# Kernel tuning notes

Measured on AMD Instinct MI355X. Metric: run time of the kernel, lower is better.

Reference implementation:

```python
import jax, jax.numpy as jnp
import numpy as np

B, L, D, V1, V2, V3 = 512, 48, 256, 512, 512, 64


def setup_inputs() -> dict:
    key = jax.random.key(0)
    ks = jax.random.split(key, 20)
    def w(k, shape, fan_in):
        return jax.random.normal(k, shape, dtype=jnp.float32) / np.sqrt(fan_in)
    inp = {
        'x1': jax.random.normal(ks[0], (B, L, V1), dtype=jnp.float32),
        'x2': jax.random.normal(ks[1], (B, L, V2), dtype=jnp.float32),
        's': jax.random.normal(ks[2], (B, V3), dtype=jnp.float32),
        'w_e1': w(ks[3], (D, V1), V1), 'b_e1': jnp.zeros((D,), jnp.float32),
        'w_e2': w(ks[4], (D, V2), V2), 'b_e2': jnp.zeros((D,), jnp.float32),
        'w_s': w(ks[5], (D, V3), V3), 'b_s': jnp.zeros((D,), jnp.float32),
        'w_x': w(ks[6], (1, D), D),                      # mlp_for_x, no bias
        'w_h': w(ks[7], (L, D), D), 'b_h': w(ks[8], (L,), D),  # mlp_for_hidden
        'w_ih': w(ks[9], (3 * D, D), D), 'w_hh': w(ks[10], (3 * D, D), D),
        'b_ih': w(ks[11], (3 * D,), D), 'b_hh': w(ks[12], (3 * D,), D),
        'w_out': w(ks[13], (1, D), D), 'b_out': jnp.zeros((1,), jnp.float32),
    }
    return inp


def _gru_cell(x, h, w_ih, w_hh, b_ih, b_hh):
    # torch GRUCell: gates ordered r, z, n
    gi = x @ w_ih.T + b_ih
    gh = h @ w_hh.T + b_hh
    i_r, i_z, i_n = jnp.split(gi, 3, axis=-1)
    h_r, h_z, h_n = jnp.split(gh, 3, axis=-1)
    r = jax.nn.sigmoid(i_r + h_r)
    z = jax.nn.sigmoid(i_z + h_z)
    n = jnp.tanh(i_n + r * h_n)
    return (1.0 - z) * n + z * h


def reference(x1, x2, s, w_e1, b_e1, w_e2, b_e2, w_s, b_s, w_x, w_h, b_h,
              w_ih, w_hh, b_ih, b_hh, w_out, b_out):
    x1e = jax.nn.relu(jnp.einsum('blv,dv->bld', x1, w_e1) + b_e1)
    x2e = jax.nn.relu(jnp.einsum('blv,dv->bld', x2, w_e2) + b_e2)
    se = s @ w_s.T + b_s                      # [B, D]
    x = x1e + x2e                             # [B, L, D]
    # prefix[:, i] = sum_{j < i} x2e[:, j, 0]  (the torch.where zero test)
    cums = jnp.cumsum(x2e[:, :, 0], axis=1)
    prefix = jnp.concatenate([jnp.zeros((B, 1), x.dtype), cums[:, :-1]], axis=1)  # [B, L]
    idx = jnp.arange(L)

    def step(h, inputs):
        i, pref = inputs                       # i: scalar step, pref: [B]
        le = (idx <= i).astype(x.dtype)        # keep timesteps 0..i (pad rest with 0)
        ip = x * le[None, :, None]             # input_padded [B, L, D]
        lt = (idx < i)
        cond = (pref == 0.0)[:, None]          # batches with zero history in ch0
        guid = jnp.where(idx[None, :] == i, 1.0,
                         jnp.where(cond & lt[None, :], 1.0, 0.0)).astype(x.dtype)  # [B, L]
        gi = ip * guid[:, :, None]
        t1 = jnp.einsum('bld,d->bl', gi, w_x[0]) + (h @ w_h.T + b_h)  # [B, L]
        a = jax.nn.softmax(t1, axis=1)
        ctx = jnp.einsum('bld,bl->bd', ip, a)
        h2 = _gru_cell(ctx, h, w_ih, w_hh, b_ih, b_hh)
        return h2, None

    h0 = jnp.zeros((B, D), x.dtype)
    hF, _ = jax.lax.scan(step, h0, (idx, prefix.T))
    y = jax.nn.sigmoid((hF + se) @ w_out.T + b_out)  # [B, 1]
    return y
```

## Files before the change

### kernel.cpp

```cpp
#include <hip/hip_runtime.h>
#include <stdint.h>

#define B_ 512
#define L_ 48
#define D_ 256

typedef __attribute__((ext_vector_type(8))) short bf16x8;
typedef __attribute__((ext_vector_type(4))) short bf16x4;
typedef __attribute__((ext_vector_type(4))) float f32x4;
typedef __attribute__((ext_vector_type(4))) int i32x4;

__device__ __forceinline__ short f2bf(float f) {
    union { float f; unsigned u; } v; v.f = f;
    unsigned u = v.u;
    unsigned r = (u + 0x7FFFu + ((u >> 16) & 1u)) >> 16;
    return (short)r;
}
__device__ __forceinline__ float bf2f(short s) {
    union { unsigned u; float f; } v; v.u = ((unsigned)(unsigned short)s) << 16;
    return v.f;
}

__global__ __launch_bounds__(256) void k_prep(const float* __restrict__ w_hh,
                                              const float* __restrict__ w_h,
                                              const float* __restrict__ w_ih,
                                              signed char* __restrict__ W1q,
                                              signed char* __restrict__ W2q,
                                              float* __restrict__ qA,
                                              float* __restrict__ qC) {
    int w = threadIdx.x >> 6, lane = threadIdx.x & 63;
    int R = blockIdx.x * 4 + w;
    if (R >= 1584) return;
    const float* src;
    signed char* dst;
    bool isA = (R < 816);
    if (R < 768)      { src = w_hh + (size_t)R * 256;         dst = W1q + (size_t)R * 256; }
    else if (R < 816) { src = w_h + (size_t)(R - 768) * 256;  dst = W1q + (size_t)R * 256; }
    else              { src = w_ih + (size_t)(R - 816) * 256; dst = W2q + (size_t)(R - 816) * 256; }
    float4 v = *(const float4*)(src + lane * 4);
    float m = fmaxf(fmaxf(fabsf(v.x), fabsf(v.y)), fmaxf(fabsf(v.z), fabsf(v.w)));
    #pragma unroll
    for (int o = 32; o; o >>= 1) m = fmaxf(m, __shfl_xor(m, o));
    float sc = (m > 0.f) ? 127.f / m : 0.f;
    int b0 = __float2int_rn(v.x * sc), b1 = __float2int_rn(v.y * sc);
    int b2 = __float2int_rn(v.z * sc), b3 = __float2int_rn(v.w * sc);
    unsigned word = (unsigned)(b0 & 255) | ((unsigned)(b1 & 255) << 8) |
                    ((unsigned)(b2 & 255) << 16) | ((unsigned)(b3 & 255) << 24);
    ((unsigned*)dst)[lane] = word;
    if (lane == 0) {
        if (isA) qA[R] = m / (127.f * 127.f);
        else     qC[R - 816] = m * 8.f / (127.f * 127.f);
    }
}

__device__ __forceinline__ void gemm_pass(const float* __restrict__ X,
                                          const float* __restrict__ W,
                                          short (*sA)[40], short (*sB)[40],
                                          int m0, int n0, int srow, int sseg,
                                          int mf, int nf, int row16, int kg,
                                          f32x4 (&acc)[2][4]) {
    for (int k0 = 0; k0 < 512; k0 += 32) {
        __syncthreads();
        {
            const float* src = X + (size_t)(m0 + srow) * 512 + k0 + sseg * 8;
            float4 p0 = *(const float4*)(src);
            float4 p1 = *(const float4*)(src + 4);
            bf16x8 v;
            v[0] = f2bf(p0.x); v[1] = f2bf(p0.y); v[2] = f2bf(p0.z); v[3] = f2bf(p0.w);
            v[4] = f2bf(p1.x); v[5] = f2bf(p1.y); v[6] = f2bf(p1.z); v[7] = f2bf(p1.w);
            *(bf16x8*)&sA[srow][sseg * 8] = v;
        }
        {
            const float* src = W + (size_t)(n0 + srow) * 512 + k0 + sseg * 8;
            float4 p0 = *(const float4*)(src);
            float4 p1 = *(const float4*)(src + 4);
            bf16x8 v;
            v[0] = f2bf(p0.x); v[1] = f2bf(p0.y); v[2] = f2bf(p0.z); v[3] = f2bf(p0.w);
            v[4] = f2bf(p1.x); v[5] = f2bf(p1.y); v[6] = f2bf(p1.z); v[7] = f2bf(p1.w);
            *(bf16x8*)&sB[srow][sseg * 8] = v;
        }
        __syncthreads();
        bf16x8 a0 = *(bf16x8*)&sA[(mf + 0) * 16 + row16][kg * 8];
        bf16x8 a1 = *(bf16x8*)&sA[(mf + 1) * 16 + row16][kg * 8];
        #pragma unroll
        for (int j = 0; j < 4; ++j) {
            bf16x8 bv = *(bf16x8*)&sB[(nf + j) * 16 + row16][kg * 8];
            acc[0][j] = __builtin_amdgcn_mfma_f32_16x16x32_bf16(a0, bv, acc[0][j], 0, 0, 0);
            acc[1][j] = __builtin_amdgcn_mfma_f32_16x16x32_bf16(a1, bv, acc[1][j], 0, 0, 0);
        }
    }
}

__device__ __forceinline__ void gemm_pass_c0(const float* __restrict__ X,
                                             const float* __restrict__ W,
                                             const float* __restrict__ we2r0,
                                             bool doC0, float& c0acc,
                                             short (*sA)[40], short (*sB)[40],
                                             int m0, int n0, int srow, int sseg,
                                             int mf, int nf, int row16, int kg,
                                             f32x4 (&acc)[2][4]) {
    for (int k0 = 0; k0 < 512; k0 += 32) {
        __syncthreads();
        {
            const float* src = X + (size_t)(m0 + srow) * 512 + k0 + sseg * 8;
            float4 p0 = *(const float4*)(src);
            float4 p1 = *(const float4*)(src + 4);
            if (doC0) {
                const float* wr = we2r0 + k0 + sseg * 8;
                c0acc += p0.x * wr[0] + p0.y * wr[1] + p0.z * wr[2] + p0.w * wr[3]
                       + p1.x * wr[4] + p1.y * wr[5] + p1.z * wr[6] + p1.w * wr[7];
            }
            bf16x8 v;
            v[0] = f2bf(p0.x); v[1] = f2bf(p0.y); v[2] = f2bf(p0.z); v[3] = f2bf(p0.w);
            v[4] = f2bf(p1.x); v[5] = f2bf(p1.y); v[6] = f2bf(p1.z); v[7] = f2bf(p1.w);
            *(bf16x8*)&sA[srow][sseg * 8] = v;
        }
        {
            const float* src = W + (size_t)(n0 + srow) * 512 + k0 + sseg * 8;
            float4 p0 = *(const float4*)(src);
            float4 p1 = *(const float4*)(src + 4);
            bf16x8 v;
            v[0] = f2bf(p0.x); v[1] = f2bf(p0.y); v[2] = f2bf(p0.z); v[3] = f2bf(p0.w);
            v[4] = f2bf(p1.x); v[5] = f2bf(p1.y); v[6] = f2bf(p1.z); v[7] = f2bf(p1.w);
            *(bf16x8*)&sB[srow][sseg * 8] = v;
        }
        __syncthreads();
        bf16x8 a0 = *(bf16x8*)&sA[(mf + 0) * 16 + row16][kg * 8];
        bf16x8 a1 = *(bf16x8*)&sA[(mf + 1) * 16 + row16][kg * 8];
        #pragma unroll
        for (int j = 0; j < 4; ++j) {
            bf16x8 bv = *(bf16x8*)&sB[(nf + j) * 16 + row16][kg * 8];
            acc[0][j] = __builtin_amdgcn_mfma_f32_16x16x32_bf16(a0, bv, acc[0][j], 0, 0, 0);
            acc[1][j] = __builtin_amdgcn_mfma_f32_16x16x32_bf16(a1, bv, acc[1][j], 0, 0, 0);
        }
    }
}

__global__ __launch_bounds__(512) void k_embed(const float* __restrict__ x1,
                                               const float* __restrict__ x2,
                                               const float* __restrict__ w_e1,
                                               const float* __restrict__ b_e1,
                                               const float* __restrict__ w_e2,
                                               const float* __restrict__ b_e2,
                                               short* __restrict__ xb,
                                               float* __restrict__ c0) {
    __shared__ short sA[128][40];
    __shared__ short sB[128][40];
    int bid = blockIdx.x;
    int mt = bid >> 1, nt = bid & 1;
    int m0 = mt * 128, n0 = nt * 128;
    int tid = threadIdx.x;
    int lane = tid & 63, w = tid >> 6;
    int mf = (w & 3) * 2;
    int nf = (w >> 2) * 4;
    int row16 = lane & 15, kg = lane >> 4;
    int srow = tid >> 2, sseg = tid & 3;

    f32x4 acc[2][4], keep[2][4];
    #pragma unroll
    for (int a = 0; a < 2; ++a)
        #pragma unroll
        for (int j = 0; j < 4; ++j) { acc[a][j] = {0.f, 0.f, 0.f, 0.f}; }

    gemm_pass(x1, w_e1, sA, sB, m0, n0, srow, sseg, mf, nf, row16, kg, acc);
    #pragma unroll
    for (int a = 0; a < 2; ++a)
        #pragma unroll
        for (int j = 0; j < 4; ++j) { keep[a][j] = acc[a][j]; acc[a][j] = {0.f, 0.f, 0.f, 0.f}; }

    float c0acc = 0.f;
    const bool doC0 = (nt == 0);
    gemm_pass_c0(x2, w_e2, w_e2, doC0, c0acc, sA, sB, m0, n0, srow, sseg, mf, nf, row16, kg, acc);

    if (doC0) {
        float t = c0acc;
        t += __shfl_xor(t, 1);
        t += __shfl_xor(t, 2);
        if (sseg == 0) c0[m0 + srow] = fmaxf(t + b_e2[0], 0.f);
    }

    #pragma unroll
    for (int a = 0; a < 2; ++a) {
        int mbase = m0 + (mf + a) * 16 + kg * 4;
        #pragma unroll
        for (int j = 0; j < 4; ++j) {
            int n = n0 + (nf + j) * 16 + row16;
            float be1 = b_e1[n], be2 = b_e2[n];
            #pragma unroll
            for (int e = 0; e < 4; ++e) {
                float v1 = fmaxf(keep[a][j][e] + be1, 0.f);
                float v2 = fmaxf(acc[a][j][e] + be2, 0.f);
                xb[(size_t)(mbase + e) * 256 + n] = f2bf(v1 + v2);
            }
        }
    }
}

__global__ __launch_bounds__(256) void k_quant(const short* __restrict__ xb,
                                               const float* __restrict__ w_x,
                                               signed char* __restrict__ xq,
                                               float* __restrict__ xs,
                                               float* __restrict__ xw) {
    int w = threadIdx.x >> 6, lane = threadIdx.x & 63;
    int row = blockIdx.x * 4 + w;
    const short* src = xb + (size_t)row * 256 + lane * 4;
    bf16x4 v = *(const bf16x4*)src;
    float f0 = bf2f(v.x), f1 = bf2f(v.y), f2 = bf2f(v.z), f3 = bf2f(v.w);
    float m = fmaxf(fmaxf(f0, f1), fmaxf(f2, f3));
    float t = f0 * w_x[lane * 4] + f1 * w_x[lane * 4 + 1] +
              f2 * w_x[lane * 4 + 2] + f3 * w_x[lane * 4 + 3];
    #pragma unroll
    for (int o = 32; o; o >>= 1) {
        m = fmaxf(m, __shfl_xor(m, o));
        t += __shfl_xor(t, o);
    }
    float sc = (m > 0.f) ? 127.f / m : 0.f;
    int b0 = __float2int_rn(f0 * sc), b1 = __float2int_rn(f1 * sc);
    int b2 = __float2int_rn(f2 * sc), b3 = __float2int_rn(f3 * sc);
    unsigned word = (unsigned)(b0 & 255) | ((unsigned)(b1 & 255) << 8) |
                    ((unsigned)(b2 & 255) << 16) | ((unsigned)(b3 & 255) << 24);
    ((unsigned*)xq)[(size_t)row * 64 + lane] = word;
    if (lane == 0) { xs[row] = m / 127.f; xw[row] = t; }
}

__global__ __launch_bounds__(256) void k_aux2(const float* __restrict__ c0,
                                              const float* __restrict__ s_in,
                                              const float* __restrict__ w_s,
                                              const float* __restrict__ b_s,
                                              unsigned long long* __restrict__ condbits,
                                              float* __restrict__ se) {
    __shared__ float sS[64];
    int b = blockIdx.x;
    int t = threadIdx.x;
    if (t < 64) sS[t] = s_in[b * 64 + t];
    __syncthreads();
    float acc = b_s[t];
    const float* wr = w_s + t * 64;
    #pragma unroll 8
    for (int kk = 0; kk < 64; ++kk) acc += sS[kk] * wr[kk];
    se[(size_t)b * 256 + t] = acc;
    if (t == 0) {
        unsigned long long bits = 0;
        bool run = true;
        const float* cr = c0 + (size_t)b * 48;
        for (int i = 0; i < 48; ++i) {
            if (run) bits |= (1ull << i);
            run = run && (cr[i] == 0.0f);
        }
        condbits[b] = bits;
    }
}

__device__ __forceinline__ void mfma4r(const i32x4 (&a)[4], const i32x4 (&b)[4], i32x4& acc) {
    #pragma unroll
    for (int s = 0; s < 4; ++s)
        acc = __builtin_amdgcn_mfma_i32_16x16x64_i8(a[s], b[s], acc, 0, 0, 0);
}

__global__ __launch_bounds__(512, 1) void k_scan(const signed char* __restrict__ W1q,
                                                 const signed char* __restrict__ W2q,
                                                 const float* __restrict__ qAg,
                                                 const float* __restrict__ qCg,
                                                 const float* __restrict__ b_hh,
                                                 const float* __restrict__ b_h,
                                                 const float* __restrict__ b_ih,
                                                 const signed char* __restrict__ xq,
                                                 const float* __restrict__ xs,
                                                 const float* __restrict__ xw,
                                                 const unsigned long long* __restrict__ condbits,
                                                 const float* __restrict__ se,
                                                 const float* __restrict__ w_out,
                                                 const float* __restrict__ b_out,
                                                 float* __restrict__ out) {
    __shared__ signed char lWc[8][3][4096];
    __shared__ signed char lWs[3][4096];
    __shared__ signed char lXqT[2][256][52];
    __shared__ signed char lH8[16][272];
    __shared__ signed char lX8[16][272];
    __shared__ float lTw[8][52];
    __shared__ float lbA[816], lqA[816], lbC[768], lqC[768];
    __shared__ float lRed[8][2];

    const int tid = threadIdx.x;
    const int w = tid >> 6, lane = tid & 63;
    const int row16 = lane & 15, kg = lane >> 4;
    const int b0 = blockIdx.x * 2;
    const int g1 = 8 + w;
    const int c0 = w * 16 + row16, c1 = g1 * 16 + row16;
    const int swz = (row16 & 7) << 4;
    const float CS = 127.f / 8.f;
    const int mb = w >> 2;
    const int dimb = ((w & 3) << 6) + lane;

    for (int t = tid; t < 816; t += 512) {
        lbA[t] = (t < 768) ? b_hh[t] : b_h[t - 768];
        lqA[t] = qAg[t];
    }
    for (int t = tid; t < 768; t += 512) { lbC[t] = b_ih[t]; lqC[t] = qCg[t]; }
    for (int t = tid; t < 1088; t += 512) {
        ((int*)lH8)[t] = 0;
        ((int*)lX8)[t] = 0;
    }
    {
        int bq = tid >> 8, dq = tid & 255;
        const signed char* src = xq + (size_t)(b0 + bq) * 12288 + dq;
        signed char* dst = &lXqT[bq][dq][0];
        #pragma unroll
        for (int j = 0; j < 48; ++j) dst[j] = src[(size_t)j * 256];
    }

    const float xwv = (lane < 48) ? xw[(size_t)(b0 + mb) * 48 + lane] : 0.f;
    const float xsv = (lane < 48) ? xs[(size_t)(b0 + mb) * 48 + lane] : 0.f;
    const float qsv = (lane < 48) ? qAg[768 + lane] : 0.f;
    const float bsv = (lane < 48) ? b_h[lane] : 0.f;
    const unsigned long long cbits = condbits[b0 + mb];

    const int fro = row16 * 256 + kg * 16;
    i32x4 wa0[3][4], wa1[3][4], wc0[3][4];
    #pragma unroll
    for (int t = 0; t < 3; ++t) {
        const signed char* p0 = W1q + (size_t)(t * 16 + w) * 4096 + fro;
        const signed char* p1 = W1q + (size_t)(t * 16 + g1) * 4096 + fro;
        const signed char* p2 = W2q + (size_t)(t * 16 + w) * 4096 + fro;
        #pragma unroll
        for (int s = 0; s < 4; ++s) {
            wa0[t][s] = *(const i32x4*)(p0 + s * 64);
            wa1[t][s] = *(const i32x4*)(p1 + s * 64);
            wc0[t][s] = *(const i32x4*)(p2 + s * 64);
        }
    }
    #pragma unroll
    for (int t = 0; t < 3; ++t) {
        const signed char* src = W2q + (size_t)(t * 16 + g1) * 4096 + fro;
        signed char* dst = &lWc[w][t][row16 * 256];
        #pragma unroll
        for (int s = 0; s < 4; ++s)
            *(i32x4*)(dst + ((kg * 16 + s * 64) ^ swz)) = *(const i32x4*)(src + s * 64);
    }
    if (w < 3) {
        const signed char* src = W1q + (size_t)(48 + w) * 4096 + fro;
        signed char* dst = &lWs[w][row16 * 256];
        #pragma unroll
        for (int s = 0; s < 4; ++s)
            *(i32x4*)(dst + ((kg * 16 + s * 64) ^ swz)) = *(const i32x4*)(src + s * 64);
    }
    __syncthreads();

    float h0[2] = {0.f, 0.f};
    float h1[2] = {0.f, 0.f};

    for (int i = 0; i < 48; ++i) {
        i32x4 av[4];
        #pragma unroll
        for (int s = 0; s < 4; ++s) av[s] = *(const i32x4*)(&lH8[row16][0] + kg * 16 + s * 64);
        i32x4 sv0 = {0,0,0,0}, sv1 = {0,0,0,0}, sv2 = {0,0,0,0};
        #pragma unroll
        for (int s = 0; s < 4; ++s) {
            int off = (kg * 16 + s * 64) ^ swz;
            i32x4 q0 = *(const i32x4*)(&lWs[0][row16 * 256] + off);
            i32x4 q1 = *(const i32x4*)(&lWs[1][row16 * 256] + off);
            i32x4 q2 = *(const i32x4*)(&lWs[2][row16 * 256] + off);
            sv0 = __builtin_amdgcn_mfma_i32_16x16x64_i8(av[s], q0, sv0, 0, 0, 0);
            sv1 = __builtin_amdgcn_mfma_i32_16x16x64_i8(av[s], q1, sv1, 0, 0, 0);
            sv2 = __builtin_amdgcn_mfma_i32_16x16x64_i8(av[s], q2, sv2, 0, 0, 0);
        }
        i32x4 aR0 = {0,0,0,0}, aZ0 = {0,0,0,0}, aN0 = {0,0,0,0};
        i32x4 aR1 = {0,0,0,0}, aZ1 = {0,0,0,0}, aN1 = {0,0,0,0};
        mfma4r(av, wa0[0], aR0); mfma4r(av, wa0[1], aZ0); mfma4r(av, wa0[2], aN0);
        mfma4r(av, wa1[0], aR1); mfma4r(av, wa1[1], aZ1); mfma4r(av, wa1[2], aN1);

        {
            float e00 = (float)sv0[0], e10 = (float)sv0[1];
            float e01 = (float)sv1[0], e11 = (float)sv1[1];
            float e02 = (float)sv2[0], e12 = (float)sv2[1];
            float s0 = mb ? e10 : e00;
            float s1 = mb ? e11 : e01;
            float s2 = mb ? e12 : e02;
            float v0 = __shfl(s0, row16);
            float v1 = __shfl(s1, row16);
            float v2 = __shfl(s2, row16);
            float raw = (lane < 16) ? v0 : ((lane < 32) ? v1 : v2);
            float val = -3.0e38f;
            if (lane < 48) {
                val = raw * qsv + bsv;
                bool cb = (cbits >> i) & 1ull;
                if (lane == i || (cb && lane < i)) val += xwv;
            }
            float mx = val;
            #pragma unroll
            for (int o = 32; o; o >>= 1) mx = fmaxf(mx, __shfl_xor(mx, o));
            float ex = (lane < 48) ? __expf(val - mx) : 0.f;
            float sm = ex;
            #pragma unroll
            for (int o = 32; o; o >>= 1) sm += __shfl_xor(sm, o);
            if (lane < 48) lTw[w][lane] = (ex / sm) * xsv;
        }
        {
            const float* tw = lTw[w];
            const signed char* xv = &lXqT[mb][dimb][0];
            float acc = 0.f;
            int j = 0;
            for (; j + 3 <= i; j += 4) {
                union { int v; signed char c[4]; } pk;
                pk.v = *(const int*)(xv + j);
                float4 t4 = *(const float4*)(tw + j);
                acc += t4.x * (float)pk.c[0] + t4.y * (float)pk.c[1]
                     + t4.z * (float)pk.c[2] + t4.w * (float)pk.c[3];
            }
            for (; j <= i; ++j) acc += tw[j] * (float)xv[j];
            lX8[mb][dimb] = (signed char)__float2int_rn(fminf(fmaxf(acc * CS, -127.f), 127.f));
        }
        __syncthreads();

        i32x4 cv[4];
        #pragma unroll
        for (int s = 0; s < 4; ++s) cv[s] = *(const i32x4*)(&lX8[row16][0] + kg * 16 + s * 64);
        {
            i32x4 cr = {0,0,0,0}, cz = {0,0,0,0}, cn = {0,0,0,0};
            mfma4r(cv, wc0[0], cr); mfma4r(cv, wc0[1], cz); mfma4r(cv, wc0[2], cn);
            #pragma unroll
            for (int e = 0; e < 2; ++e) {
                float gr = (float)aR0[e] * lqA[c0]       + lbA[c0]       + (float)cr[e] * lqC[c0]       + lbC[c0];
                float gz = (float)aZ0[e] * lqA[256 + c0] + lbA[256 + c0] + (float)cz[e] * lqC[256 + c0] + lbC[256 + c0];
                float gh = (float)aN0[e] * lqA[512 + c0] + lbA[512 + c0];
                float gn = (float)cn[e] * lqC[512 + c0]  + lbC[512 + c0];
                float r = 1.f / (1.f + __expf(-gr));
                float z = 1.f / (1.f + __expf(-gz));
                float nn = 1.f - 2.f / (__expf(2.f * (gn + r * gh)) + 1.f);
                float hp = (1.f - z) * nn + z * h0[e];
                h0[e] = hp;
                if (kg == 0)
                    lH8[e][c0] = (signed char)__float2int_rn(fminf(fmaxf(hp, -1.f), 1.f) * 127.f);
            }
        }
        {
            i32x4 cr = {0,0,0,0}, cz = {0,0,0,0}, cn = {0,0,0,0};
            #pragma unroll
            for (int s = 0; s < 4; ++s) {
                int off = (kg * 16 + s * 64) ^ swz;
                i32x4 br = *(const i32x4*)(&lWc[w][0][row16 * 256] + off);
                i32x4 bz = *(const i32x4*)(&lWc[w][1][row16 * 256] + off);
                i32x4 bn = *(const i32x4*)(&lWc[w][2][row16 * 256] + off);
                cr = __builtin_amdgcn_mfma_i32_16x16x64_i8(cv[s], br, cr, 0, 0, 0);
                cz = __builtin_amdgcn_mfma_i32_16x16x64_i8(cv[s], bz, cz, 0, 0, 0);
                cn = __builtin_amdgcn_mfma_i32_16x16x64_i8(cv[s], bn, cn, 0, 0, 0);
            }
            #pragma unroll
            for (int e = 0; e < 2; ++e) {
                float gr = (float)aR1[e] * lqA[c1]       + lbA[c1]       + (float)cr[e] * lqC[c1]       + lbC[c1];
                float gz = (float)aZ1[e] * lqA[256 + c1] + lbA[256 + c1] + (float)cz[e] * lqC[256 + c1] + lbC[256 + c1];
                float gh = (float)aN1[e] * lqA[512 + c1] + lbA[512 + c1];
                float gn = (float)cn[e] * lqC[512 + c1]  + lbC[512 + c1];
                float r = 1.f / (1.f + __expf(-gr));
                float z = 1.f / (1.f + __expf(-gz));
                float nn = 1.f - 2.f / (__expf(2.f * (gn + r * gh)) + 1.f);
                float hp = (1.f - z) * nn + z * h1[e];
                h1[e] = hp;
                if (kg == 0)
                    lH8[e][c1] = (signed char)__float2int_rn(fminf(fmaxf(hp, -1.f), 1.f) * 127.f);
            }
        }
        __syncthreads();
    }

    if (kg == 0) {
        float p[2];
        #pragma unroll
        for (int e = 0; e < 2; ++e) {
            int b = b0 + e;
            p[e] = (h0[e] + se[(size_t)b * 256 + c0]) * w_out[c0]
                 + (h1[e] + se[(size_t)b * 256 + c1]) * w_out[c1];
        }
        #pragma unroll
        for (int o = 1; o < 16; o <<= 1) {
            #pragma unroll
            for (int e = 0; e < 2; ++e) p[e] += __shfl_xor(p[e], o);
        }
        if (row16 == 0) {
            #pragma unroll
            for (int e = 0; e < 2; ++e) lRed[w][e] = p[e];
        }
    }
    __syncthreads();
    if (tid < 2) {
        float sum = 0.f;
        #pragma unroll
        for (int q = 0; q < 8; ++q) sum += lRed[q][tid];
        out[b0 + tid] = 1.f / (1.f + __expf(-(sum + b_out[0])));
    }
}

extern "C" void kernel_launch(void* const* d_in, const int* in_sizes, int n_in,
                              void* d_out, int out_size, void* d_ws, size_t ws_size,
                              hipStream_t stream) {
    const float* x1   = (const float*)d_in[0];
    const float* x2   = (const float*)d_in[1];
    const float* s    = (const float*)d_in[2];
    const float* w_e1 = (const float*)d_in[3];
    const float* b_e1 = (const float*)d_in[4];
    const float* w_e2 = (const float*)d_in[5];
    const float* b_e2 = (const float*)d_in[6];
    const float* w_s  = (const float*)d_in[7];
    const float* b_s  = (const float*)d_in[8];
    const float* w_x  = (const float*)d_in[9];
    const float* w_h  = (const float*)d_in[10];
    const float* b_h  = (const float*)d_in[11];
    const float* w_ih = (const float*)d_in[12];
    const float* w_hh = (const float*)d_in[13];
    const float* b_ih = (const float*)d_in[14];
    const float* b_hh = (const float*)d_in[15];
    const float* w_out = (const float*)d_in[16];
    const float* b_out = (const float*)d_in[17];
    float* out = (float*)d_out;

    char* ws = (char*)d_ws;
    size_t off = 0;
    auto alloc = [&](size_t bytes) -> void* {
        void* p = ws + off;
        off = (off + bytes + 255) & ~(size_t)255;
        return p;
    };
    short* xb = (short*)alloc((size_t)B_ * L_ * D_ * 2);
    signed char* xq = (signed char*)alloc((size_t)B_ * L_ * D_);
    float* xs = (float*)alloc((size_t)B_ * L_ * 4);
    signed char* W1q = (signed char*)alloc(896 * 256);
    signed char* W2q = (signed char*)alloc(768 * 256);
    float* qA = (float*)alloc(816 * 4);
    float* qC = (float*)alloc(768 * 4);
    float* c0 = (float*)alloc((size_t)B_ * L_ * 4);
    float* xw = (float*)alloc((size_t)B_ * L_ * 4);
    unsigned long long* cb = (unsigned long long*)alloc(B_ * 8);
    float* se = (float*)alloc((size_t)B_ * D_ * 4);

    hipLaunchKernelGGL(k_prep, dim3(396), dim3(256), 0, stream,
                       w_hh, w_h, w_ih, W1q, W2q, qA, qC);
    hipLaunchKernelGGL(k_embed, dim3(384), dim3(512), 0, stream,
                       x1, x2, w_e1, b_e1, w_e2, b_e2, xb, c0);
    hipLaunchKernelGGL(k_quant, dim3(6144), dim3(256), 0, stream,
                       xb, w_x, xq, xs, xw);
    hipLaunchKernelGGL(k_aux2, dim3(512), dim3(256), 0, stream,
                       c0, s, w_s, b_s, cb, se);
    hipLaunchKernelGGL(k_scan, dim3(256), dim3(512), 0, stream,
                       W1q, W2q, qA, qC, b_hh, b_h, b_ih, xq, xs, xw, cb, se,
                       w_out, b_out, out);
}
```

Baseline: 231.2 us.

## Compute attention context with int8 MFMA and keep gate scales in registers

Each wave now runs the softmax for both batch rows, quantizes the attention weights to int8 with a per-row max scale, and computes the context vector with int8 MFMA against the transposed x tile. This replaces the scalar per-thread dot-product loop over timesteps. Per-column gate biases and scales are also hoisted from LDS into registers. The cost is duplicated softmax work across all waves, extra quantization error from int8 attention weights, and higher register pressure.

```diff
diff --git a/kernel.cpp b/kernel.cpp
--- a/kernel.cpp
+++ b/kernel.cpp
@@ -274,11 +274,10 @@
                                                  float* __restrict__ out) {
     __shared__ signed char lWc[8][3][4096];
     __shared__ signed char lWs[3][4096];
-    __shared__ signed char lXqT[2][256][52];
+    __shared__ signed char lXqT[2][256][64];
     __shared__ signed char lH8[16][272];
     __shared__ signed char lX8[16][272];
-    __shared__ float lTw[8][52];
-    __shared__ float lbA[816], lqA[816], lbC[768], lqC[768];
+    __shared__ signed char lAq[8][2][64];
     __shared__ float lRed[8][2];
 
     const int tid = threadIdx.x;
@@ -289,31 +288,38 @@
     const int c0 = w * 16 + row16, c1 = g1 * 16 + row16;
     const int swz = (row16 & 7) << 4;
     const float CS = 127.f / 8.f;
-    const int mb = w >> 2;
-    const int dimb = ((w & 3) << 6) + lane;
-
-    for (int t = tid; t < 816; t += 512) {
-        lbA[t] = (t < 768) ? b_hh[t] : b_h[t - 768];
-        lqA[t] = qAg[t];
-    }
-    for (int t = tid; t < 768; t += 512) { lbC[t] = b_ih[t]; lqC[t] = qCg[t]; }
+
     for (int t = tid; t < 1088; t += 512) {
         ((int*)lH8)[t] = 0;
         ((int*)lX8)[t] = 0;
     }
+    if (tid < 256) ((int*)lAq)[tid] = 0;
     {
         int bq = tid >> 8, dq = tid & 255;
         const signed char* src = xq + (size_t)(b0 + bq) * 12288 + dq;
         signed char* dst = &lXqT[bq][dq][0];
         #pragma unroll
         for (int j = 0; j < 48; ++j) dst[j] = src[(size_t)j * 256];
-    }
-
-    const float xwv = (lane < 48) ? xw[(size_t)(b0 + mb) * 48 + lane] : 0.f;
-    const float xsv = (lane < 48) ? xs[(size_t)(b0 + mb) * 48 + lane] : 0.f;
+        *(int4*)(dst + 48) = (int4){0, 0, 0, 0};
+    }
+
+    const float xwv0 = (lane < 48) ? xw[(size_t)b0 * 48 + lane] : 0.f;
+    const float xwv1 = (lane < 48) ? xw[(size_t)(b0 + 1) * 48 + lane] : 0.f;
+    const float xsv0 = (lane < 48) ? xs[(size_t)b0 * 48 + lane] : 0.f;
+    const float xsv1 = (lane < 48) ? xs[(size_t)(b0 + 1) * 48 + lane] : 0.f;
     const float qsv = (lane < 48) ? qAg[768 + lane] : 0.f;
     const float bsv = (lane < 48) ? b_h[lane] : 0.f;
-    const unsigned long long cbits = condbits[b0 + mb];
+    const unsigned long long cb0 = condbits[b0];
+    const unsigned long long cb1 = condbits[b0 + 1];
+
+    const float qA0r = qAg[c0], qA0z = qAg[256 + c0], qA0n = qAg[512 + c0];
+    const float bA0r = b_hh[c0], bA0z = b_hh[256 + c0], bA0n = b_hh[512 + c0];
+    const float qC0r = qCg[c0], qC0z = qCg[256 + c0], qC0n = qCg[512 + c0];
+    const float bC0r = b_ih[c0], bC0z = b_ih[256 + c0], bC0n = b_ih[512 + c0];
+    const float qA1r = qAg[c1], qA1z = qAg[256 + c1], qA1n = qAg[512 + c1];
+    const float bA1r = b_hh[c1], bA1z = b_hh[256 + c1], bA1n = b_hh[512 + c1];
+    const float qC1r = qCg[c1], qC1z = qCg[256 + c1], qC1n = qCg[512 + c1];
+    const float bC1r = b_ih[c1], bC1z = b_ih[256 + c1], bC1n = b_ih[512 + c1];
 
     const int fro = row16 * 256 + kg * 16;
     i32x4 wa0[3][4], wa1[3][4], wc0[3][4];
@@ -348,6 +354,7 @@
 
     float h0[2] = {0.f, 0.f};
     float h1[2] = {0.f, 0.f};
+    float ascale0 = 0.f, ascale1 = 0.f;
 
     for (int i = 0; i < 48; ++i) {
         i32x4 av[4];
@@ -369,46 +376,61 @@
         mfma4r(av, wa0[0], aR0); mfma4r(av, wa0[1], aZ0); mfma4r(av, wa0[2], aN0);
         mfma4r(av, wa1[0], aR1); mfma4r(av, wa1[1], aZ1); mfma4r(av, wa1[2], aN1);
 
-        {
-            float e00 = (float)sv0[0], e10 = (float)sv0[1];
-            float e01 = (float)sv1[0], e11 = (float)sv1[1];
-            float e02 = (float)sv2[0], e12 = (float)sv2[1];
-            float s0 = mb ? e10 : e00;
-            float s1 = mb ? e11 : e01;
-            float s2 = mb ? e12 : e02;
-            float v0 = __shfl(s0, row16);
-            float v1 = __shfl(s1, row16);
-            float v2 = __shfl(s2, row16);
-            float raw = (lane < 16) ? v0 : ((lane < 32) ? v1 : v2);
-            float val = -3.0e38f;
-            if (lane < 48) {
-                val = raw * qsv + bsv;
-                bool cb = (cbits >> i) & 1ull;
-                if (lane == i || (cb && lane < i)) val += xwv;
+        #define SOFTMAX_REP(E, XWV, XSV, CB, ASC)                                   \
+        {                                                                           \
+            float s0 = (float)sv0[E], s1_ = (float)sv1[E], s2_ = (float)sv2[E];     \
+            float v0 = __shfl(s0, row16);                                           \
+            float v1 = __shfl(s1_, row16);                                          \
+            float v2 = __shfl(s2_, row16);                                          \
+            float raw = (lane < 16) ? v0 : ((lane < 32) ? v1 : v2);                 \
+            float val = -3.0e38f;                                                   \
+            if (lane < 48) {                                                        \
+                val = raw * qsv + bsv;                                              \
+                bool cb = (CB >> i) & 1ull;                                         \
+                if (lane == i || (cb && lane < i)) val += XWV;                      \
+            }                                                                       \
+            float mx = val;                                                         \
+            _Pragma("unroll")                                                       \
+            for (int o = 32; o; o >>= 1) mx = fmaxf(mx, __shfl_xor(mx, o));         \
+            float ex = (lane < 48) ? __expf(val - mx) : 0.f;                        \
+            float pvs = ex * XSV;                                                   \
+            float sm = ex, mp = pvs;                                                \
+            _Pragma("unroll")                                                       \
+            for (int o = 32; o; o >>= 1) {                                          \
+                sm += __shfl_xor(sm, o);                                            \
+                mp = fmaxf(mp, __shfl_xor(mp, o));                                  \
+            }                                                                       \
+            float rqn = (mp > 0.f) ? 127.f / mp : 0.f;                              \
+            int ai = __float2int_rn(pvs * rqn);                                     \
+            if (lane < 48) lAq[w][E][lane] = (signed char)ai;                       \
+            ASC = mp / (127.f * sm);                                                \
+        }
+        SOFTMAX_REP(0, xwv0, xsv0, cb0, ascale0)
+        SOFTMAX_REP(1, xwv1, xsv1, cb1, ascale1)
+        #undef SOFTMAX_REP
+
+        {
+            i32x4 ba0 = *(const i32x4*)(&lAq[w][0][kg * 16]);
+            i32x4 ba1 = *(const i32x4*)(&lAq[w][1][kg * 16]);
+            #pragma unroll
+            for (int tt = 0; tt < 2; ++tt) {
+                const int dt = (w * 2 + tt) * 16;
+                i32x4 xa0 = *(const i32x4*)(&lXqT[0][dt + row16][kg * 16]);
+                i32x4 xa1 = *(const i32x4*)(&lXqT[1][dt + row16][kg * 16]);
+                i32x4 zc = {0, 0, 0, 0};
+                i32x4 c0v = __builtin_amdgcn_mfma_i32_16x16x64_i8(xa0, ba0, zc, 0, 0, 0);
+                i32x4 c1v = __builtin_amdgcn_mfma_i32_16x16x64_i8(xa1, ba1, zc, 0, 0, 0);
+                if (row16 == 0) {
+                    #pragma unroll
+                    for (int e = 0; e < 4; ++e) {
+                        int d = dt + kg * 4 + e;
+                        float f0 = (float)c0v[e] * ascale0 * CS;
+                        float f1 = (float)c1v[e] * ascale1 * CS;
+                        lX8[0][d] = (signed char)__float2int_rn(fminf(fmaxf(f0, -127.f), 127.f));
+                        lX8[1][d] = (signed char)__float2int_rn(fminf(fmaxf(f1, -127.f), 127.f));
+                    }
+                }
             }
-            float mx = val;
-            #pragma unroll
-            for (int o = 32; o; o >>= 1) mx = fmaxf(mx, __shfl_xor(mx, o));
-            float ex = (lane < 48) ? __expf(val - mx) : 0.f;
-            float sm = ex;
-            #pragma unroll
-            for (int o = 32; o; o >>= 1) sm += __shfl_xor(sm, o);
-            if (lane < 48) lTw[w][lane] = (ex / sm) * xsv;
-        }
-        {
-            const float* tw = lTw[w];
-            const signed char* xv = &lXqT[mb][dimb][0];
-            float acc = 0.f;
-            int j = 0;
-            for (; j + 3 <= i; j += 4) {
-                union { int v; signed char c[4]; } pk;
-                pk.v = *(const int*)(xv + j);
-                float4 t4 = *(const float4*)(tw + j);
-                acc += t4.x * (float)pk.c[0] + t4.y * (float)pk.c[1]
-                     + t4.z * (float)pk.c[2] + t4.w * (float)pk.c[3];
-            }
-            for (; j <= i; ++j) acc += tw[j] * (float)xv[j];
-            lX8[mb][dimb] = (signed char)__float2int_rn(fminf(fmaxf(acc * CS, -127.f), 127.f));
         }
         __syncthreads();
 
@@ -420,10 +442,10 @@
             mfma4r(cv, wc0[0], cr); mfma4r(cv, wc0[1], cz); mfma4r(cv, wc0[2], cn);
             #pragma unroll
             for (int e = 0; e < 2; ++e) {
-                float gr = (float)aR0[e] * lqA[c0]       + lbA[c0]       + (float)cr[e] * lqC[c0]       + lbC[c0];
-                float gz = (float)aZ0[e] * lqA[256 + c0] + lbA[256 + c0] + (float)cz[e] * lqC[256 + c0] + lbC[256 + c0];
-                float gh = (float)aN0[e] * lqA[512 + c0] + lbA[512 + c0];
-                float gn = (float)cn[e] * lqC[512 + c0]  + lbC[512 + c0];
+                float gr = (float)aR0[e] * qA0r + bA0r + (float)cr[e] * qC0r + bC0r;
+                float gz = (float)aZ0[e] * qA0z + bA0z + (float)cz[e] * qC0z + bC0z;
+                float gh = (float)aN0[e] * qA0n + bA0n;
+                float gn = (float)cn[e] * qC0n + bC0n;
                 float r = 1.f / (1.f + __expf(-gr));
                 float z = 1.f / (1.f + __expf(-gz));
                 float nn = 1.f - 2.f / (__expf(2.f * (gn + r * gh)) + 1.f);
@@ -447,10 +469,10 @@
             }
             #pragma unroll
             for (int e = 0; e < 2; ++e) {
-                float gr = (float)aR1[e] * lqA[c1]       + lbA[c1]       + (float)cr[e] * lqC[c1]       + lbC[c1];
-                float gz = (float)aZ1[e] * lqA[256 + c1] + lbA[256 + c1] + (float)cz[e] * lqC[256 + c1] + lbC[256 + c1];
-                float gh = (float)aN1[e] * lqA[512 + c1] + lbA[512 + c1];
-                float gn = (float)cn[e] * lqC[512 + c1]  + lbC[512 + c1];
+                float gr = (float)aR1[e] * qA1r + bA1r + (float)cr[e] * qC1r + bC1r;
+                float gz = (float)aZ1[e] * qA1z + bA1z + (float)cz[e] * qC1z + bC1z;
+                float gh = (float)aN1[e] * qA1n + bA1n;
+                float gn = (float)cn[e] * qC1n + bC1n;
                 float r = 1.f / (1.f + __expf(-gr));
                 float z = 1.f / (1.f + __expf(-gz));
                 float nn = 1.f - 2.f / (__expf(2.f * (gn + r * gh)) + 1.f);
```

New measurement: 267.4 us. 15.7% more time.
